# Kernel optimization log

Measured on AMD Instinct MI355X. Metric: run time of the kernel, lower is better.

## Reference

```python
import jax, jax.numpy as jnp
import numpy as np

N = 262144   # number of samples
C = 16       # GMM components
D = 64       # feature dim


def setup_inputs() -> dict:
    key = jax.random.key(0)
    k1, k2, k3, k4 = jax.random.split(key, 4)
    inputs = jax.random.normal(k1, (N, D), dtype=jnp.float32)
    # SPD inverse covariances, as produced by inverting fitted GMM covariances
    R = jax.random.normal(k2, (C, D, D), dtype=jnp.float32)
    covariances_inv = jnp.einsum('cij,ckj->cik', R, R) / D + 0.1 * jnp.eye(D, dtype=jnp.float32)
    means = jax.random.normal(k3, (C, D), dtype=jnp.float32)
    w = jax.random.uniform(k4, (C,), dtype=jnp.float32, minval=0.1, maxval=1.0)
    weights = w / jnp.sum(w)  # mixture weights sum to 1
    return {"inputs": inputs, "covariances_inv": covariances_inv,
            "means": means, "weights": weights}


def reference(inputs, covariances_inv, means, weights):
    # Mahalanobis quadratic form per component: d[n,c] = (x_n - m_c)^T Sigma_c^{-1} (x_n - m_c)
    centered = inputs[:, None, :] - means[None, :, :]                # [N, C, D]
    distances_sqr = jnp.einsum('ncd,cde,nce->nc', centered, covariances_inv, centered)  # [N, C]
    # score_n = prod_c d[n,c] ** w_c
    score = jnp.prod(distances_sqr ** weights[None, :], axis=1)      # [N]
    return score
```

## Files before the change

### kernel.cpp

```cpp
#include <hip/hip_runtime.h>

typedef __attribute__((ext_vector_type(4))) float f32x4;
typedef __attribute__((ext_vector_type(8))) short bf16x8;

__device__ __forceinline__ short f2bf(float f) {
    union { float f; unsigned u; } v; v.f = f;
    unsigned u = v.u + 0x7FFFu + ((v.u >> 16) & 1u);
    return (short)(u >> 16);
}
__device__ __forceinline__ int pack_bf2(float a, float b) {
    union { float f; unsigned u; } ua, ub; ua.f = a; ub.f = b;
    unsigned x = ua.u + 0x8000u, y = ub.u + 0x8000u;
    return (int)__builtin_amdgcn_perm(y, x, 0x07060302u);
}
__device__ __forceinline__ float bflo(int p) {
    union { int i; float f; } v; v.i = p << 16; return v.f;
}
__device__ __forceinline__ float bfhi(int p) {
    union { int i; float f; } v; v.i = p & 0xffff0000; return v.f;
}

#if __has_builtin(__builtin_amdgcn_permlane16_swap) && \
    __has_builtin(__builtin_amdgcn_permlane32_swap)
__device__ __forceinline__ float quad_sum(float dp) {
    unsigned u = __float_as_uint(dp);
    auto r1 = __builtin_amdgcn_permlane16_swap(u, u, false, false);
    float s = __uint_as_float(r1[0]) + __uint_as_float(r1[1]);
    unsigned v = __float_as_uint(s);
    auto r2 = __builtin_amdgcn_permlane32_swap(v, v, false, false);
    return __uint_as_float(r2[0]) + __uint_as_float(r2[1]);
}
#else
__device__ __forceinline__ float quad_sum(float dp) {
    dp += __shfl_xor(dp, 16, 64);
    dp += __shfl_xor(dp, 32, 64);
    return dp;
}
#endif

__global__ void gmm_prep(const float* __restrict__ Ainv,
                         const float* __restrict__ means,
                         short* __restrict__ AbP16,
                         float* __restrict__ biasP,
                         float* __restrict__ kscal) {
    __shared__ float sA[64 * 68];
    __shared__ float sm[64];
    __shared__ float sb[64];
    const int c = blockIdx.x, t = threadIdx.x;
    const float* A = Ainv + c * 4096;
    #pragma unroll
    for (int i = 0; i < 4; ++i) {
        int flat = i * 1024 + t * 4;
        int r = flat >> 6, col = flat & 63;
        *(f32x4*)&sA[r * 68 + col] = *(const f32x4*)(A + flat);
    }
    if (t < 64) sm[t] = means[c * 64 + t];
    __syncthreads();
    {
        int j = t >> 2, seg = t & 3;
        float p = 0.f;
        #pragma unroll
        for (int k = 0; k < 16; ++k) p += sA[j * 68 + seg * 16 + k] * sm[seg * 16 + k];
        p += __shfl_xor(p, 1, 64); p += __shfl_xor(p, 2, 64);
        if ((t & 3) == 0) sb[j] = p;
    }
    __syncthreads();
    if (t < 64) {
        float km = sm[t] * sb[t];
        #pragma unroll
        for (int off = 32; off >= 1; off >>= 1) km += __shfl_xor(km, off, 64);
        if (t == 0) kscal[c] = km;
        int rt = t >> 4, qh = (t >> 2) & 3, r = t & 3;
        int pj = (rt >> 1) * 32 + 8 * qh + 4 * (rt & 1) + r;
        biasP[c * 64 + t] = -2.f * sb[pj];
    }
    #pragma unroll
    for (int rep = 0; rep < 2; ++rep) {
        int f = rep * 256 + t;
        int rt = f >> 7, kc = (f >> 6) & 1, L = f & 63;
        int ln = L & 15, q = L >> 4;
        int pj = (rt >> 1) * 32 + 8 * (ln >> 2) + 4 * (rt & 1) + (ln & 3);
        const float* src = &sA[pj * 68 + 32 * kc + 8 * q];
        bf16x8 v;
        #pragma unroll
        for (int j = 0; j < 8; ++j) v[j] = f2bf(src[j]);
        *(bf16x8*)(AbP16 + c * 4096 + f * 8) = v;
    }
}

union BFrag { bf16x8 v; int i[4]; };

__global__ __launch_bounds__(256) void gmm_main(
    const float* __restrict__ X,
    const float* __restrict__ weights,
    const short* __restrict__ AbP16,
    const float* __restrict__ biasP,
    const float* __restrict__ kscal,
    float* __restrict__ out) {

    __shared__ short sAb[16384];
    __shared__ float sBias[16 * 64];
    __shared__ float sKW[32];

    const int tid = threadIdx.x;
    const int lane = tid & 63, w = tid >> 6;
    const int q = lane >> 4, ln = lane & 15;
    const int base = blockIdx.x * 256 + w * 64;

    #pragma unroll
    for (int i = 0; i < 8; ++i)
        ((int4*)sAb)[i * 256 + tid] = ((const int4*)AbP16)[i * 256 + tid];
    ((f32x4*)sBias)[tid] = ((const f32x4*)biasP)[tid];
    if (tid < 16) { sKW[tid] = kscal[tid]; sKW[16 + tid] = weights[tid]; }

    BFrag xb[4][2];
    #pragma unroll
    for (int t = 0; t < 4; ++t) {
        const float* xr = X + (size_t)(base + t * 16 + ln) * 64 + 8 * q;
        #pragma unroll
        for (int kc = 0; kc < 2; ++kc) {
            f32x4 a = *(const f32x4*)(xr + 32 * kc);
            f32x4 b = *(const f32x4*)(xr + 32 * kc + 4);
            xb[t][kc].i[0] = pack_bf2(a[0], a[1]);
            xb[t][kc].i[1] = pack_bf2(a[2], a[3]);
            xb[t][kc].i[2] = pack_bf2(b[0], b[1]);
            xb[t][kc].i[3] = pack_bf2(b[2], b[3]);
        }
    }
    __syncthreads();

    float slog[4] = {0.f, 0.f, 0.f, 0.f};

    #pragma unroll 1
    for (int g = 0; g < 4; ++g) {
        #pragma unroll 1
        for (int cl = 0; cl < 4; ++cl) {
            const int c = g * 4 + cl;
            bf16x8 af[8];
            #pragma unroll
            for (int f = 0; f < 8; ++f)
                af[f] = *(const bf16x8*)&sAb[cl * 4096 + f * 512 + lane * 8];
            f32x4 bias[4];
            #pragma unroll
            for (int rt = 0; rt < 4; ++rt)
                bias[rt] = *(const f32x4*)&sBias[c * 64 + rt * 16 + q * 4];
            const float kc_ = sKW[c], wcc = sKW[16 + c];

            #pragma unroll
            for (int t = 0; t < 4; ++t) {
                float dp0 = 0.f, dp1 = 0.f;
                #pragma unroll
                for (int rt = 0; rt < 4; ++rt) {
                    f32x4 acc = __builtin_amdgcn_mfma_f32_16x16x32_bf16(
                        af[rt * 2 + 0], xb[t][0].v, bias[rt], 0, 0, 0);
                    acc = __builtin_amdgcn_mfma_f32_16x16x32_bf16(
                        af[rt * 2 + 1], xb[t][1].v, acc, 0, 0, 0);
                    int pa = xb[t][rt >> 1].i[(rt & 1) * 2];
                    int pb = xb[t][rt >> 1].i[(rt & 1) * 2 + 1];
                    float pr = acc[0] * bflo(pa) + acc[1] * bfhi(pa)
                             + acc[2] * bflo(pb) + acc[3] * bfhi(pb);
                    if (rt & 1) dp1 += pr; else dp0 += pr;
                }
                float dp = quad_sum(dp0 + dp1);
                float d = fmaxf(dp + kc_, 1e-30f);
                slog[t] = fmaf(wcc, __builtin_amdgcn_logf(d), slog[t]);
            }
        }
        if (g < 3) {
            __syncthreads();
            const int4* src = (const int4*)(AbP16 + (g + 1) * 16384);
            #pragma unroll
            for (int i = 0; i < 8; ++i)
                ((int4*)sAb)[i * 256 + tid] = src[i * 256 + tid];
            __syncthreads();
        }
    }

    float s0 = (q & 1) ? slog[1] : slog[0];
    float s1 = (q & 1) ? slog[3] : slog[2];
    float sv = (q & 2) ? s1 : s0;
    out[base + lane] = __builtin_amdgcn_exp2f(sv);
}

extern "C" void kernel_launch(void* const* d_in, const int* in_sizes, int n_in,
                              void* d_out, int out_size, void* d_ws, size_t ws_size,
                              hipStream_t stream) {
    const float* X       = (const float*)d_in[0];
    const float* Ainv    = (const float*)d_in[1];
    const float* means   = (const float*)d_in[2];
    const float* weights = (const float*)d_in[3];
    float* out = (float*)d_out;
    const int N = in_sizes[0] / 64;

    short* AbP16 = (short*)d_ws;
    float* biasP = (float*)((char*)d_ws + 131072);
    float* kscal = (float*)((char*)d_ws + 135168);

    gmm_prep<<<dim3(16), dim3(256), 0, stream>>>(Ainv, means, AbP16, biasP, kscal);
    gmm_main<<<dim3(N / 256), dim3(256), 0, stream>>>(X, weights, AbP16, biasP, kscal, out);
}
```

Before: 129.4 us.

## Load precision-matrix fragments directly from global memory instead of LDS staging

Drops the shared-memory staging of the per-component bf16 matrices, bias and scalars, along with the block barriers. Each wave now reads its MFMA A-fragments, bias and scalars straight from global memory, relying on L1/L2 caching of the small 128KB table, and iterates all 16 components in one loop. Launch bounds now request 4 blocks per SM. This removes the LDS copies and syncs, which should raise occupancy, but each wave pays global-memory latency per component and no longer shares the loads within the block.

```diff
diff --git a/kernel.cpp b/kernel.cpp
--- a/kernel.cpp
+++ b/kernel.cpp
@@ -90,7 +90,7 @@
 
 union BFrag { bf16x8 v; int i[4]; };
 
-__global__ __launch_bounds__(256) void gmm_main(
+__global__ __launch_bounds__(256, 4) void gmm_main(
     const float* __restrict__ X,
     const float* __restrict__ weights,
     const short* __restrict__ AbP16,
@@ -98,20 +98,10 @@
     const float* __restrict__ kscal,
     float* __restrict__ out) {
 
-    __shared__ short sAb[16384];
-    __shared__ float sBias[16 * 64];
-    __shared__ float sKW[32];
-
     const int tid = threadIdx.x;
     const int lane = tid & 63, w = tid >> 6;
     const int q = lane >> 4, ln = lane & 15;
     const int base = blockIdx.x * 256 + w * 64;
-
-    #pragma unroll
-    for (int i = 0; i < 8; ++i)
-        ((int4*)sAb)[i * 256 + tid] = ((const int4*)AbP16)[i * 256 + tid];
-    ((f32x4*)sBias)[tid] = ((const f32x4*)biasP)[tid];
-    if (tid < 16) { sKW[tid] = kscal[tid]; sKW[16 + tid] = weights[tid]; }
 
     BFrag xb[4][2];
     #pragma unroll
@@ -127,52 +117,40 @@
             xb[t][kc].i[3] = pack_bf2(b[2], b[3]);
         }
     }
-    __syncthreads();
 
     float slog[4] = {0.f, 0.f, 0.f, 0.f};
 
     #pragma unroll 1
-    for (int g = 0; g < 4; ++g) {
-        #pragma unroll 1
-        for (int cl = 0; cl < 4; ++cl) {
-            const int c = g * 4 + cl;
-            bf16x8 af[8];
+    for (int c = 0; c < 16; ++c) {
+        const short* aP = AbP16 + c * 4096 + lane * 8;
+        bf16x8 af[8];
+        #pragma unroll
+        for (int f = 0; f < 8; ++f)
+            af[f] = *(const bf16x8*)(aP + f * 512);
+        f32x4 bias[4];
+        #pragma unroll
+        for (int rt = 0; rt < 4; ++rt)
+            bias[rt] = *(const f32x4*)(biasP + c * 64 + rt * 16 + q * 4);
+        const float kc_ = kscal[c], wcc = weights[c];
+
+        #pragma unroll
+        for (int t = 0; t < 4; ++t) {
+            float dp0 = 0.f, dp1 = 0.f;
             #pragma unroll
-            for (int f = 0; f < 8; ++f)
-                af[f] = *(const bf16x8*)&sAb[cl * 4096 + f * 512 + lane * 8];
-            f32x4 bias[4];
-            #pragma unroll
-            for (int rt = 0; rt < 4; ++rt)
-                bias[rt] = *(const f32x4*)&sBias[c * 64 + rt * 16 + q * 4];
-            const float kc_ = sKW[c], wcc = sKW[16 + c];
-
-            #pragma unroll
-            for (int t = 0; t < 4; ++t) {
-                float dp0 = 0.f, dp1 = 0.f;
-                #pragma unroll
-                for (int rt = 0; rt < 4; ++rt) {
-                    f32x4 acc = __builtin_amdgcn_mfma_f32_16x16x32_bf16(
-                        af[rt * 2 + 0], xb[t][0].v, bias[rt], 0, 0, 0);
-                    acc = __builtin_amdgcn_mfma_f32_16x16x32_bf16(
-                        af[rt * 2 + 1], xb[t][1].v, acc, 0, 0, 0);
-                    int pa = xb[t][rt >> 1].i[(rt & 1) * 2];
-                    int pb = xb[t][rt >> 1].i[(rt & 1) * 2 + 1];
-                    float pr = acc[0] * bflo(pa) + acc[1] * bfhi(pa)
-                             + acc[2] * bflo(pb) + acc[3] * bfhi(pb);
-                    if (rt & 1) dp1 += pr; else dp0 += pr;
-                }
-                float dp = quad_sum(dp0 + dp1);
-                float d = fmaxf(dp + kc_, 1e-30f);
-                slog[t] = fmaf(wcc, __builtin_amdgcn_logf(d), slog[t]);
+            for (int rt = 0; rt < 4; ++rt) {
+                f32x4 acc = __builtin_amdgcn_mfma_f32_16x16x32_bf16(
+                    af[rt * 2 + 0], xb[t][0].v, bias[rt], 0, 0, 0);
+                acc = __builtin_amdgcn_mfma_f32_16x16x32_bf16(
+                    af[rt * 2 + 1], xb[t][1].v, acc, 0, 0, 0);
+                int pa = xb[t][rt >> 1].i[(rt & 1) * 2];
+                int pb = xb[t][rt >> 1].i[(rt & 1) * 2 + 1];
+                float pr = acc[0] * bflo(pa) + acc[1] * bfhi(pa)
+                         + acc[2] * bflo(pb) + acc[3] * bfhi(pb);
+                if (rt & 1) dp1 += pr; else dp0 += pr;
             }
-        }
-        if (g < 3) {
-            __syncthreads();
-            const int4* src = (const int4*)(AbP16 + (g + 1) * 16384);
-            #pragma unroll
-            for (int i = 0; i < 8; ++i)
-                ((int4*)sAb)[i * 256 + tid] = src[i * 256 + tid];
-            __syncthreads();
+            float dp = quad_sum(dp0 + dp1);
+            float d = fmaxf(dp + kc_, 1e-30f);
+            slog[t] = fmaf(wcc, __builtin_amdgcn_logf(d), slog[t]);
         }
     }
 
```

Result: no change. 128.8 us (-0.4%).
